# Kernel tuning notes

Hardware: AMD Instinct MI355X
Metric: run time of the kernel (lower is better)

The kernel has to match this reference:

```python
import jax, jax.numpy as jnp
import numpy as np

B, L, S, H, E, D = 8, 1024, 1024, 8, 64, 64


def setup_inputs() -> dict:
    key = jax.random.key(0)
    kq, kk, kv, ka = jax.random.split(key, 4)
    queries = jax.random.normal(kq, (B, L, H, E), dtype=jnp.float32)
    keys = jax.random.normal(kk, (B, S, H, E), dtype=jnp.float32)
    values = jax.random.normal(kv, (B, S, H, D), dtype=jnp.float32)
    # previous layer's attention logits (residual bias), scaled down a bit
    A = jax.random.normal(ka, (B, H, L, S), dtype=jnp.float32) * 0.1
    # causal mask: True = masked (strict upper triangle), shape (B,1,L,S)
    attn_mask = jnp.broadcast_to(
        jnp.triu(jnp.ones((L, S), dtype=bool), k=1)[None, None], (B, 1, L, S)
    )
    return {"queries": queries, "keys": keys, "values": values,
            "attn_mask": attn_mask, "A": A}


def reference(queries, keys, values, attn_mask, A):
    # queries: (B,L,H,E), keys/values: (B,S,H,E/D), A: (B,H,L,S)
    E_ = queries.shape[-1]
    scale = 1.0 / jnp.sqrt(jnp.asarray(E_, dtype=queries.dtype))
    scores = jnp.einsum('blhe,bshe->bhls', queries, keys)  # (B,H,L,S)
    neg_inf = jnp.asarray(-jnp.inf, dtype=scores.dtype)
    scores = jnp.where(attn_mask, neg_inf, scores)
    # layer_nums > 0: residual bias from previous layer's logits
    A_new = jax.nn.softmax(scale * scores + A, axis=-1)
    # dropout p=0.0 -> identity (eval-mode reference)
    V = jnp.einsum('bhls,bshd->blhd', A_new, values)  # (B,L,H,D)
    return V, A_new
```

## Files before the change

### kernel.cpp

```cpp
#include <hip/hip_runtime.h>

#define B_ 8
#define L_ 1024
#define S_ 1024
#define H_ 8
#define E_ 64
#define D_ 64

typedef __attribute__((ext_vector_type(8))) short bf16x8;
typedef __attribute__((ext_vector_type(4))) short bf16x4;
typedef __attribute__((ext_vector_type(4))) float f32x4;
typedef __attribute__((ext_vector_type(4))) ushort u16x4;

__device__ __forceinline__ ushort f2b(float f) {
    unsigned u = __float_as_uint(f);
    return (ushort)((u + 0x7fffu + ((u >> 16) & 1u)) >> 16);
}
__device__ __forceinline__ float b2f(ushort b) {
    return __uint_as_float(((unsigned)b) << 16);
}

#if __has_builtin(__builtin_amdgcn_mfma_f32_16x16x16bf16_1k)
__device__ __forceinline__ f32x4 mfma16(bf16x4 a, bf16x4 b, f32x4 c) {
    return __builtin_amdgcn_mfma_f32_16x16x16bf16_1k(a, b, c, 0, 0, 0);
}
#elif __has_builtin(__builtin_amdgcn_mfma_f32_16x16x16_bf16)
__device__ __forceinline__ f32x4 mfma16(bf16x4 a, bf16x4 b, f32x4 c) {
    return __builtin_amdgcn_mfma_f32_16x16x16_bf16(a, b, c, 0, 0, 0);
}
#else
__device__ __forceinline__ f32x4 mfma16(bf16x4 a, bf16x4 b, f32x4 c) {
    f32x4 d;
    asm("v_mfma_f32_16x16x16_bf16 %0, %1, %2, %3" : "=v"(d) : "v"(a), "v"(b), "v"(c));
    return d;
}
#endif

__device__ __forceinline__ bf16x8 load8_f2b(const float* p) {
    float4 a = *(const float4*)(p);
    float4 b = *(const float4*)(p + 4);
    bf16x8 r;
    r[0] = (short)f2b(a.x); r[1] = (short)f2b(a.y);
    r[2] = (short)f2b(a.z); r[3] = (short)f2b(a.w);
    r[4] = (short)f2b(b.x); r[5] = (short)f2b(b.y);
    r[6] = (short)f2b(b.z); r[7] = (short)f2b(b.w);
    return r;
}

__global__ __launch_bounds__(256) void vt_kernel(const float* __restrict__ V,
                                                 ushort* __restrict__ VT) {
    __shared__ ushort tile[64][72];
    int bh = blockIdx.x >> 4;
    int st = blockIdx.x & 15;
    int t  = threadIdx.x;
    int b = bh >> 3, h = bh & 7;

    int s_loc = t >> 2;
    int dg = (t & 3) << 4;
    const float* src = V + (((size_t)(b * S_ + st * 64 + s_loc) * H_ + h) * D_ + dg);
#pragma unroll
    for (int v = 0; v < 4; ++v) {
        float4 f = *(const float4*)(src + v * 4);
        tile[s_loc][dg + v * 4 + 0] = f2b(f.x);
        tile[s_loc][dg + v * 4 + 1] = f2b(f.y);
        tile[s_loc][dg + v * 4 + 2] = f2b(f.z);
        tile[s_loc][dg + v * 4 + 3] = f2b(f.w);
    }
    __syncthreads();

    int d = t >> 2;
    int sg = (t & 3) << 4;
    ushort tmp[16];
#pragma unroll
    for (int i = 0; i < 16; ++i) tmp[i] = tile[sg + i][d];
    ushort* dst = VT + (((size_t)bh * D_ + d) * S_ + st * 64 + sg);
    *(uint4*)(dst)     = *(uint4*)&tmp[0];
    *(uint4*)(dst + 8) = *(uint4*)&tmp[8];
}

__global__ __launch_bounds__(256) void kb_kernel(const float* __restrict__ K,
                                                 ushort* __restrict__ KB) {
    size_t i = ((size_t)blockIdx.x * 256 + threadIdx.x) * 8;
    float4 a = *(const float4*)(K + i);
    float4 b = *(const float4*)(K + i + 4);
    ushort o[8];
    o[0] = f2b(a.x); o[1] = f2b(a.y); o[2] = f2b(a.z); o[3] = f2b(a.w);
    o[4] = f2b(b.x); o[5] = f2b(b.y); o[6] = f2b(b.z); o[7] = f2b(b.w);
    *(uint4*)(KB + i) = *(uint4*)o;
}

template <int USE_WS>
__global__ __launch_bounds__(256, 5) void attn_kernel(
    const float* __restrict__ Q, const float* __restrict__ K,
    const float* __restrict__ A, const ushort* __restrict__ KB,
    const ushort* __restrict__ VT, const float* __restrict__ V,
    float* __restrict__ outV, float* __restrict__ outA) {
    __shared__ float red[4][16];
    __shared__ float obuf[4][16][66];

    int idx  = blockIdx.x;
    int lt   = 63 - (idx & 63);
    int bh   = idx >> 6;
    int b    = bh >> 3, h = bh & 7;
    int l0   = lt << 4;
    int t    = threadIdx.x;
    int wave = t >> 6, lane = t & 63;
    int quad = lane >> 4, lm = lane & 15;

    const size_t qbase = ((size_t)(b * L_ + l0 + lm) * H_ + h) * E_ + quad * 8;
    bf16x8 qf0 = load8_f2b(Q + qbase);
    bf16x8 qf1 = load8_f2b(Q + qbase + 32);

    const float scale = 0.125f;
    int nsb = lt + 1;
    int rg  = l0 + lm;
    const float* Arow = A + ((size_t)bh * L_ + l0 + lm) * S_ + quad * 4;
    const ushort* VTrow = VT + ((size_t)bh * D_ + lm) * S_;

    float psum = 0.f;
    u16x4 stash[16];
    f32x4 oacc[4] = {{0.f,0.f,0.f,0.f},{0.f,0.f,0.f,0.f},{0.f,0.f,0.f,0.f},{0.f,0.f,0.f,0.f}};
#pragma unroll
    for (int i = 0; i < 16; ++i) {
        int sb = wave + i * 4;
        if (sb < nsb) {
            int s0 = sb << 4;
            int c0 = s0 + quad * 4;
            const size_t kbase = ((size_t)(b * S_ + s0 + lm) * H_ + h) * E_ + quad * 8;
            bf16x8 kf0, kf1;
            if (USE_WS) {
                kf0 = *(const bf16x8*)(KB + kbase);
                kf1 = *(const bf16x8*)(KB + kbase + 32);
            } else {
                kf0 = load8_f2b(K + kbase);
                kf1 = load8_f2b(K + kbase + 32);
            }
            float4 a4 = *(const float4*)(Arow + s0);
            f32x4 acc = {0.f, 0.f, 0.f, 0.f};
            acc = __builtin_amdgcn_mfma_f32_16x16x32_bf16(kf0, qf0, acc, 0, 0, 0);
            acc = __builtin_amdgcn_mfma_f32_16x16x32_bf16(kf1, qf1, acc, 0, 0, 0);
            u16x4 ps;
            bf16x4 pf;
#pragma unroll
            for (int r = 0; r < 4; ++r) {
                float av = (r == 0) ? a4.x : (r == 1) ? a4.y : (r == 2) ? a4.z : a4.w;
                float z = acc[r] * scale + av;
                float p = (c0 + r <= rg) ? __expf(z) : 0.f;
                psum += p;
                ps[r] = f2b(p);
                pf[r] = (short)ps[r];
            }
            stash[i] = ps;
#pragma unroll
            for (int dd = 0; dd < 4; ++dd) {
                bf16x4 vf;
                if (USE_WS) {
                    u16x4 vr = *(const u16x4*)(VTrow + (size_t)dd * 16 * S_ + c0);
                    vf[0] = (short)vr[0]; vf[1] = (short)vr[1];
                    vf[2] = (short)vr[2]; vf[3] = (short)vr[3];
                } else {
#pragma unroll
                    for (int j = 0; j < 4; ++j)
                        vf[j] = (short)f2b(V[((size_t)(b * S_ + c0 + j) * H_ + h) * D_ + dd * 16 + lm]);
                }
                oacc[dd] = mfma16(pf, vf, oacc[dd]);
            }
        }
    }

    psum += __shfl_xor(psum, 16);
    psum += __shfl_xor(psum, 32);
    if (quad == 0) red[wave][lm] = psum;
#pragma unroll
    for (int dd = 0; dd < 4; ++dd)
#pragma unroll
        for (int r = 0; r < 4; ++r)
            obuf[wave][quad * 4 + r][dd * 16 + lm] = oacc[dd][r];
    __syncthreads();

    float invA = 1.0f / (red[0][lm] + red[1][lm] + red[2][lm] + red[3][lm]);
    float* Aout = outA + ((size_t)bh * L_ + l0 + lm) * S_ + quad * 4;
#pragma unroll
    for (int i = 0; i < 16; ++i) {
        int sb = wave + i * 4;
        int s0 = sb << 4;
        float4 o;
        if (sb < nsb) {
            u16x4 ps = stash[i];
            o.x = b2f(ps[0]) * invA;
            o.y = b2f(ps[1]) * invA;
            o.z = b2f(ps[2]) * invA;
            o.w = b2f(ps[3]) * invA;
        } else {
            o = make_float4(0.f, 0.f, 0.f, 0.f);
        }
        *(float4*)(Aout + s0) = o;
    }

#pragma unroll
    for (int i = 0; i < 4; ++i) {
        int slot = t + i * 256;
        int l = slot >> 6, d = slot & 63;
        float sum = obuf[0][l][d] + obuf[1][l][d] + obuf[2][l][d] + obuf[3][l][d];
        float inv = 1.0f / (red[0][l] + red[1][l] + red[2][l] + red[3][l]);
        outV[((size_t)(b * L_ + l0 + l) * H_ + h) * D_ + d] = sum * inv;
    }
}

extern "C" void kernel_launch(void* const* d_in, const int* in_sizes, int n_in,
                              void* d_out, int out_size, void* d_ws, size_t ws_size,
                              hipStream_t stream) {
    const float* Q = (const float*)d_in[0];
    const float* K = (const float*)d_in[1];
    const float* V = (const float*)d_in[2];
    const float* A = (const float*)d_in[4];
    float* outV = (float*)d_out;
    float* outA = outV + (size_t)B_ * L_ * H_ * D_;

    size_t vt_elems = (size_t)B_ * H_ * D_ * S_;
    size_t kb_elems = (size_t)B_ * S_ * H_ * E_;
    size_t need = (vt_elems + kb_elems) * sizeof(ushort);
    ushort* VT = (ushort*)d_ws;
    ushort* KB = VT + vt_elems;

    if (ws_size >= need) {
        vt_kernel<<<B_ * H_ * (S_ / 64), 256, 0, stream>>>(V, VT);
        kb_kernel<<<(int)(kb_elems / (256 * 8)), 256, 0, stream>>>(K, KB);
        attn_kernel<1><<<B_ * H_ * (L_ / 16), 256, 0, stream>>>(Q, K, A, KB, VT, V, outV, outA);
    } else {
        attn_kernel<0><<<B_ * H_ * (L_ / 16), 256, 0, stream>>>(Q, K, A, KB, VT, V, outV, outA);
    }
}
```

Measured before the change: 661.3 us.

## Prefetch next K/A/V fragments and coalesce A output writes through LDS

Adds software pipelining to the attention loop: the K, A-bias and V^T fragments for the next S-block are loaded before the current block's MFMAs and exp run, hiding global load latency. The A_new output store is restructured so that bf16 probabilities are staged in shared memory and each wave writes full contiguous 1 KB row segments, replacing strided 16-byte writes scattered across rows. The occupancy hint drops from 5 to 4 blocks per SIMD to make room for the extra prefetch registers. Extra syncthreads and LDS round trips are added in the epilogue.

```diff
diff --git a/kernel.cpp b/kernel.cpp
--- a/kernel.cpp
+++ b/kernel.cpp
@@ -89,14 +89,20 @@
     *(uint4*)(KB + i) = *(uint4*)o;
 }
 
+struct Frag {
+    bf16x8 kf0, kf1;
+    float4 a4;
+    u16x4  vr0, vr1, vr2, vr3;
+};
+
 template <int USE_WS>
-__global__ __launch_bounds__(256, 5) void attn_kernel(
+__global__ __launch_bounds__(256, 4) void attn_kernel(
     const float* __restrict__ Q, const float* __restrict__ K,
     const float* __restrict__ A, const ushort* __restrict__ KB,
     const ushort* __restrict__ VT, const float* __restrict__ V,
     float* __restrict__ outV, float* __restrict__ outA) {
     __shared__ float red[4][16];
-    __shared__ float obuf[4][16][66];
+    __shared__ __align__(16) float obuf[4][16][66];
 
     int idx  = blockIdx.x;
     int lt   = 63 - (idx & 63);
@@ -114,36 +120,59 @@
     const float scale = 0.125f;
     int nsb = lt + 1;
     int rg  = l0 + lm;
-    const float* Arow = A + ((size_t)bh * L_ + l0 + lm) * S_ + quad * 4;
+    const float* Arow = A + ((size_t)bh * L_ + l0 + lm) * S_;
     const ushort* VTrow = VT + ((size_t)bh * D_ + lm) * S_;
+
+    auto load_frag = [&](int sb) {
+        Frag f;
+        int s0 = sb << 4;
+        int c0 = s0 + quad * 4;
+        const size_t kbase = ((size_t)(b * S_ + s0 + lm) * H_ + h) * E_ + quad * 8;
+        if (USE_WS) {
+            f.kf0 = *(const bf16x8*)(KB + kbase);
+            f.kf1 = *(const bf16x8*)(KB + kbase + 32);
+        } else {
+            f.kf0 = load8_f2b(K + kbase);
+            f.kf1 = load8_f2b(K + kbase + 32);
+        }
+        f.a4 = *(const float4*)(Arow + c0);
+        if (USE_WS) {
+            f.vr0 = *(const u16x4*)(VTrow + (size_t)0 * 16 * S_ + c0);
+            f.vr1 = *(const u16x4*)(VTrow + (size_t)1 * 16 * S_ + c0);
+            f.vr2 = *(const u16x4*)(VTrow + (size_t)2 * 16 * S_ + c0);
+            f.vr3 = *(const u16x4*)(VTrow + (size_t)3 * 16 * S_ + c0);
+        } else {
+            u16x4 vr[4];
+#pragma unroll
+            for (int dd = 0; dd < 4; ++dd)
+#pragma unroll
+                for (int j = 0; j < 4; ++j)
+                    vr[dd][j] = f2b(V[((size_t)(b * S_ + c0 + j) * H_ + h) * D_ + dd * 16 + lm]);
+            f.vr0 = vr[0]; f.vr1 = vr[1]; f.vr2 = vr[2]; f.vr3 = vr[3];
+        }
+        return f;
+    };
 
     float psum = 0.f;
     u16x4 stash[16];
     f32x4 oacc[4] = {{0.f,0.f,0.f,0.f},{0.f,0.f,0.f,0.f},{0.f,0.f,0.f,0.f},{0.f,0.f,0.f,0.f}};
+    Frag cur, nxt;
+    if (wave < nsb) cur = load_frag(wave);
 #pragma unroll
     for (int i = 0; i < 16; ++i) {
-        int sb = wave + i * 4;
+        int sb  = wave + i * 4;
+        int sbn = sb + 4;
+        if (sbn < nsb) nxt = load_frag(sbn);
         if (sb < nsb) {
-            int s0 = sb << 4;
-            int c0 = s0 + quad * 4;
-            const size_t kbase = ((size_t)(b * S_ + s0 + lm) * H_ + h) * E_ + quad * 8;
-            bf16x8 kf0, kf1;
-            if (USE_WS) {
-                kf0 = *(const bf16x8*)(KB + kbase);
-                kf1 = *(const bf16x8*)(KB + kbase + 32);
-            } else {
-                kf0 = load8_f2b(K + kbase);
-                kf1 = load8_f2b(K + kbase + 32);
-            }
-            float4 a4 = *(const float4*)(Arow + s0);
+            int c0 = (sb << 4) + quad * 4;
             f32x4 acc = {0.f, 0.f, 0.f, 0.f};
-            acc = __builtin_amdgcn_mfma_f32_16x16x32_bf16(kf0, qf0, acc, 0, 0, 0);
-            acc = __builtin_amdgcn_mfma_f32_16x16x32_bf16(kf1, qf1, acc, 0, 0, 0);
+            acc = __builtin_amdgcn_mfma_f32_16x16x32_bf16(cur.kf0, qf0, acc, 0, 0, 0);
+            acc = __builtin_amdgcn_mfma_f32_16x16x32_bf16(cur.kf1, qf1, acc, 0, 0, 0);
             u16x4 ps;
             bf16x4 pf;
 #pragma unroll
             for (int r = 0; r < 4; ++r) {
-                float av = (r == 0) ? a4.x : (r == 1) ? a4.y : (r == 2) ? a4.z : a4.w;
+                float av = (r == 0) ? cur.a4.x : (r == 1) ? cur.a4.y : (r == 2) ? cur.a4.z : cur.a4.w;
                 float z = acc[r] * scale + av;
                 float p = (c0 + r <= rg) ? __expf(z) : 0.f;
                 psum += p;
@@ -151,21 +180,18 @@
                 pf[r] = (short)ps[r];
             }
             stash[i] = ps;
-#pragma unroll
-            for (int dd = 0; dd < 4; ++dd) {
-                bf16x4 vf;
-                if (USE_WS) {
-                    u16x4 vr = *(const u16x4*)(VTrow + (size_t)dd * 16 * S_ + c0);
-                    vf[0] = (short)vr[0]; vf[1] = (short)vr[1];
-                    vf[2] = (short)vr[2]; vf[3] = (short)vr[3];
-                } else {
-#pragma unroll
-                    for (int j = 0; j < 4; ++j)
-                        vf[j] = (short)f2b(V[((size_t)(b * S_ + c0 + j) * H_ + h) * D_ + dd * 16 + lm]);
-                }
-                oacc[dd] = mfma16(pf, vf, oacc[dd]);
+            bf16x4 v0, v1, v2, v3;
+#pragma unroll
+            for (int j = 0; j < 4; ++j) {
+                v0[j] = (short)cur.vr0[j]; v1[j] = (short)cur.vr1[j];
+                v2[j] = (short)cur.vr2[j]; v3[j] = (short)cur.vr3[j];
             }
-        }
+            oacc[0] = mfma16(pf, v0, oacc[0]);
+            oacc[1] = mfma16(pf, v1, oacc[1]);
+            oacc[2] = mfma16(pf, v2, oacc[2]);
+            oacc[3] = mfma16(pf, v3, oacc[3]);
+        }
+        cur = nxt;
     }
 
     psum += __shfl_xor(psum, 16);
@@ -177,25 +203,6 @@
         for (int r = 0; r < 4; ++r)
             obuf[wave][quad * 4 + r][dd * 16 + lm] = oacc[dd][r];
     __syncthreads();
-
-    float invA = 1.0f / (red[0][lm] + red[1][lm] + red[2][lm] + red[3][lm]);
-    float* Aout = outA + ((size_t)bh * L_ + l0 + lm) * S_ + quad * 4;
-#pragma unroll
-    for (int i = 0; i < 16; ++i) {
-        int sb = wave + i * 4;
-        int s0 = sb << 4;
-        float4 o;
-        if (sb < nsb) {
-            u16x4 ps = stash[i];
-            o.x = b2f(ps[0]) * invA;
-            o.y = b2f(ps[1]) * invA;
-            o.z = b2f(ps[2]) * invA;
-            o.w = b2f(ps[3]) * invA;
-        } else {
-            o = make_float4(0.f, 0.f, 0.f, 0.f);
-        }
-        *(float4*)(Aout + s0) = o;
-    }
 
 #pragma unroll
     for (int i = 0; i < 4; ++i) {
@@ -204,6 +211,39 @@
         float sum = obuf[0][l][d] + obuf[1][l][d] + obuf[2][l][d] + obuf[3][l][d];
         float inv = 1.0f / (red[0][l] + red[1][l] + red[2][l] + red[3][l]);
         outV[((size_t)(b * L_ + l0 + l) * H_ + h) * D_ + d] = sum * inv;
+    }
+
+    float invA[4];
+#pragma unroll
+    for (int r = 0; r < 4; ++r) {
+        int R = wave * 4 + r;
+        invA[r] = 1.0f / (red[0][R] + red[1][R] + red[2][R] + red[3][R]);
+    }
+    ushort* cb = (ushort*)&obuf[0][0][0];
+#pragma unroll
+    for (int c = 0; c < 4; ++c) {
+        __syncthreads();
+#pragma unroll
+        for (int j = 0; j < 4; ++j) {
+            int i  = c * 4 + j;
+            int sb = wave + i * 4;
+            int lb = wave + 4 * j;
+            u16x4 ps = {0, 0, 0, 0};
+            if (sb < nsb) ps = stash[i];
+            *(u16x4*)&cb[lm * 264 + lb * 16 + quad * 4] = ps;
+        }
+        __syncthreads();
+#pragma unroll
+        for (int r = 0; r < 4; ++r) {
+            int R = wave * 4 + r;
+            u16x4 pv = *(const u16x4*)&cb[R * 264 + lane * 4];
+            float4 o;
+            o.x = b2f(pv[0]) * invA[r];
+            o.y = b2f(pv[1]) * invA[r];
+            o.z = b2f(pv[2]) * invA[r];
+            o.w = b2f(pv[3]) * invA[r];
+            *(float4*)(outA + ((size_t)bh * L_ + l0 + R) * S_ + c * 256 + lane * 4) = o;
+        }
     }
 }
 
```

Result: faster. 622.1 us (-5.9%).
